# Kernel tuning notes

Hardware: AMD Instinct MI355X
Metric: run time of the kernel (lower is better)

## Reference

```python
import jax, jax.numpy as jnp
import numpy as np

B, S, H = 2, 2048, 2048
NH, KVH, HD = 16, 4, 128
R = 16
LORA_SCALE = 32.0 / 16.0  # lora_alpha / lora_r
ATTN_SCALE = HD ** -0.5
NEG = -1e9


def setup_inputs() -> dict:
    key = jax.random.key(0)
    ks = jax.random.split(key, 16)
    q_dim, kv_dim = NH * HD, KVH * HD
    # RoPE tables
    inv_freq = 1.0 / (10000.0 ** (jnp.arange(0, HD, 2, dtype=jnp.float32) / HD))
    ang = jnp.arange(S, dtype=jnp.float32)[:, None] * inv_freq[None, :]  # [S, HD/2]
    emb = jnp.concatenate([ang, ang], axis=-1)  # [S, HD]
    cos = jnp.broadcast_to(jnp.cos(emb)[None], (B, S, HD))
    sin = jnp.broadcast_to(jnp.sin(emb)[None], (B, S, HD))
    # additive causal mask [B,1,S,S]
    causal = jnp.triu(jnp.full((S, S), NEG, dtype=jnp.float32), k=1)
    attention_mask = jnp.broadcast_to(causal[None, None], (B, 1, S, S))
    return {
        'hidden_states': jax.random.normal(ks[0], (B, S, H), jnp.float32),
        'cos': cos,
        'sin': sin,
        'attention_mask': attention_mask,
        'q_w': jax.random.normal(ks[1], (q_dim, H), jnp.float32) * 0.02,
        'k_w': jax.random.normal(ks[2], (kv_dim, H), jnp.float32) * 0.02,
        'v_w': jax.random.normal(ks[3], (kv_dim, H), jnp.float32) * 0.02,
        'q_b': jax.random.normal(ks[4], (q_dim,), jnp.float32) * 0.02,
        'k_b': jax.random.normal(ks[5], (kv_dim,), jnp.float32) * 0.02,
        'v_b': jax.random.normal(ks[6], (kv_dim,), jnp.float32) * 0.02,
        'q_A': jax.random.normal(ks[7], (H, R), jnp.float32) * (1.0 / np.sqrt(H)),
        'q_B': jax.random.normal(ks[8], (R, q_dim), jnp.float32) * 0.02,
        'k_A': jax.random.normal(ks[9], (H, R), jnp.float32) * (1.0 / np.sqrt(H)),
        'k_B': jax.random.normal(ks[10], (R, kv_dim), jnp.float32) * 0.02,
        'v_A': jax.random.normal(ks[11], (H, R), jnp.float32) * (1.0 / np.sqrt(H)),
        'v_B': jax.random.normal(ks[12], (R, kv_dim), jnp.float32) * 0.02,
        'o_w': jax.random.normal(ks[13], (H, H), jnp.float32) * 0.02,
    }


def _rotate_half(x):
    x1, x2 = x[..., : HD // 2], x[..., HD // 2:]
    return jnp.concatenate([-x2, x1], axis=-1)


def reference(hidden_states, cos, sin, attention_mask,
              q_w, k_w, v_w, q_b, k_b, v_b,
              q_A, q_B, k_A, k_B, v_A, v_B, o_w):
    x = hidden_states  # dropout p=0 (eval)
    # fused base + LoRA projections
    q = x @ q_w.T + q_b + LORA_SCALE * ((x @ q_A) @ q_B)  # [B,S,NH*HD]
    k = x @ k_w.T + k_b + LORA_SCALE * ((x @ k_A) @ k_B)  # [B,S,KVH*HD]
    v = x @ v_w.T + v_b + LORA_SCALE * ((x @ v_A) @ v_B)
    q = q.reshape(B, S, NH, HD).transpose(0, 2, 1, 3)   # [B,NH,S,HD]
    k = k.reshape(B, S, KVH, HD).transpose(0, 2, 1, 3)  # [B,KVH,S,HD]
    v = v.reshape(B, S, KVH, HD).transpose(0, 2, 1, 3)
    # RoPE
    c = cos[:, None]  # [B,1,S,HD]
    s = sin[:, None]
    q = q * c + _rotate_half(q) * s
    k = k * c + _rotate_half(k) * s
    # GQA: repeat kv heads
    n_rep = NH // KVH
    k = jnp.repeat(k, n_rep, axis=1)  # [B,NH,S,HD]
    v = jnp.repeat(v, n_rep, axis=1)
    scores = jnp.einsum('bhqd,bhkd->bhqk', q, k) * ATTN_SCALE
    scores = scores + attention_mask
    attn = jax.nn.softmax(scores.astype(jnp.float32), axis=-1).astype(q.dtype)
    out = jnp.einsum('bhqk,bhkd->bhqd', attn, v)
    out = out.transpose(0, 2, 1, 3).reshape(B, S, NH * HD)  # [B,S,H]
    return out @ o_w.T
```

## Files before the change

### kernel.cpp

```cpp
#include <hip/hip_runtime.h>

constexpr int cB   = 2;
constexpr int cS   = 2048;
constexpr int cH   = 2048;
constexpr int cNH  = 16;
constexpr int cKVH = 4;
constexpr int cHD  = 128;
constexpr int cQD  = 2048;
constexpr int cKVD = 512;
constexpr int cNQKV = 3072;
constexpr int cNTOK = 4096;
#define ATTN_SCALE 0.08838834764831845f

typedef __bf16 bf16;
typedef __attribute__((ext_vector_type(8))) __bf16 bf16x8;
typedef __attribute__((ext_vector_type(4))) __bf16 bf16x4;
typedef __attribute__((ext_vector_type(4))) float  f32x4;

__device__ __forceinline__ void async_load16(const bf16* g, bf16* l) {
    __builtin_amdgcn_global_load_lds(
        (const __attribute__((address_space(1))) void*)g,
        (__attribute__((address_space(3))) void*)l, 16, 0, 0);
}

__global__ void conv_f32_bf16(const float* __restrict__ in, bf16* __restrict__ out) {
    int i = (blockIdx.x * 256 + threadIdx.x) * 4;
    f32x4 v = *(const f32x4*)(in + i);
    bf16x4 o;
    o[0] = (bf16)v[0]; o[1] = (bf16)v[1]; o[2] = (bf16)v[2]; o[3] = (bf16)v[3];
    *(bf16x4*)(out + i) = o;
}

__global__ void prep_w(const float* __restrict__ qw, const float* __restrict__ kw, const float* __restrict__ vw,
                       const float* __restrict__ qA, const float* __restrict__ qB,
                       const float* __restrict__ kA, const float* __restrict__ kB,
                       const float* __restrict__ vA, const float* __restrict__ vB,
                       bf16* __restrict__ Wc) {
    const int idx = blockIdx.x * 256 + threadIdx.x;
    const int n = idx >> 11, k = idx & 2047;
    const float* W; const float* Am; const float* Bm; int nn, nd;
    if (n < cQD)             { W = qw; Am = qA; Bm = qB; nn = n;          nd = cQD; }
    else if (n < cQD + cKVD) { W = kw; Am = kA; Bm = kB; nn = n - cQD;    nd = cKVD; }
    else                     { W = vw; Am = vA; Bm = vB; nn = n - cQD - cKVD; nd = cKVD; }
    float acc = 0.f;
    #pragma unroll
    for (int r = 0; r < 16; ++r) acc += Am[k * 16 + r] * Bm[r * nd + nn];
    Wc[(size_t)n * cH + k] = (bf16)(W[(size_t)nn * cH + k] + 2.0f * acc);
}

__global__ void prep_bias(const float* __restrict__ qb, const float* __restrict__ kb,
                          const float* __restrict__ vb, float* __restrict__ biasc) {
    int n = blockIdx.x * 256 + threadIdx.x;
    if (n >= cNQKV) return;
    biasc[n] = (n < cQD) ? qb[n] : (n < cQD + cKVD ? kb[n - cQD] : vb[n - cQD - cKVD]);
}

template <int OUTF32>
__global__ __launch_bounds__(256) void gemm_bt(const bf16* __restrict__ A, const bf16* __restrict__ Bw,
                                               const float* __restrict__ bias, void* __restrict__ Cp,
                                               int M, int N, int K) {
    __shared__ bf16 Al[128 * 32];
    __shared__ bf16 Bl[128 * 32];
    const int tid = threadIdx.x;
    const int wave = tid >> 6, lane = tid & 63;
    const int quad = lane >> 4, l16 = lane & 15;
    const int wr = wave >> 1, wc = wave & 1;
    const long bm = (long)blockIdx.y * 128, bn = (long)blockIdx.x * 128;

    f32x4 acc[4][4];
    #pragma unroll
    for (int i = 0; i < 4; ++i)
        #pragma unroll
        for (int c = 0; c < 4; ++c) acc[i][c] = f32x4{0.f, 0.f, 0.f, 0.f};

    const int r0 = lane >> 2;
    const int kc = (lane & 3) * 8;

    for (int k0 = 0; k0 < K; k0 += 32) {
        __syncthreads();
        #pragma unroll
        for (int j = 0; j < 2; ++j) {
            const int rb = (wave * 2 + j) * 16;
            const int row = rb + r0;
            async_load16(A  + (size_t)(bm + row) * K + k0 + kc, &Al[rb * 32 + r0 * 32 + kc]);
            async_load16(Bw + (size_t)(bn + row) * K + k0 + kc, &Bl[rb * 32 + r0 * 32 + kc]);
        }
        __syncthreads();
        bf16x8 af[4], bfr[4];
        #pragma unroll
        for (int i = 0; i < 4; ++i) af[i]  = *(const bf16x8*)&Al[(wr * 64 + i * 16 + l16) * 32 + quad * 8];
        #pragma unroll
        for (int c = 0; c < 4; ++c) bfr[c] = *(const bf16x8*)&Bl[(wc * 64 + c * 16 + l16) * 32 + quad * 8];
        #pragma unroll
        for (int i = 0; i < 4; ++i)
            #pragma unroll
            for (int c = 0; c < 4; ++c)
                acc[i][c] = __builtin_amdgcn_mfma_f32_16x16x32_bf16(af[i], bfr[c], acc[i][c], 0, 0, 0);
    }

    #pragma unroll
    for (int i = 0; i < 4; ++i)
        #pragma unroll
        for (int c = 0; c < 4; ++c) {
            const long m0 = bm + wr * 64 + i * 16 + quad * 4;
            const long n  = bn + wc * 64 + c * 16 + l16;
            #pragma unroll
            for (int r = 0; r < 4; ++r) {
                float v = acc[i][c][r];
                if (OUTF32) {
                    ((float*)Cp)[(m0 + r) * N + n] = v;
                } else {
                    v += bias[n];
                    ((bf16*)Cp)[(m0 + r) * N + n] = (bf16)v;
                }
            }
        }
}

__global__ void rope_reorder(const bf16* __restrict__ Y, const float* __restrict__ cosb,
                             const float* __restrict__ sinb,
                             bf16* __restrict__ Qr, bf16* __restrict__ Kr) {
    const int c = blockIdx.x * 256 + threadIdx.x;
    const int t = blockIdx.y;
    const int b = t >> 11, s = t & 2047;
    const int hh = c >> 6, dl = c & 63;
    const int col = hh * 128 + dl;
    const size_t yrow = (size_t)t * cNQKV;
    float y1 = (float)Y[yrow + col];
    float y2 = (float)Y[yrow + col + 64];
    float cv = cosb[(size_t)t * cHD + dl];
    float sv = sinb[(size_t)t * cHD + dl];
    float o1 = y1 * cv - y2 * sv;
    float o2 = y2 * cv + y1 * sv;
    if (hh < cNH) {
        o1 *= ATTN_SCALE; o2 *= ATTN_SCALE;
        bf16* dst = Qr + ((size_t)(b * cNH + hh) * cS + s) * cHD + dl;
        dst[0]  = (bf16)o1;
        dst[64] = (bf16)o2;
    } else {
        bf16* dst = Kr + ((size_t)(b * cKVH + (hh - cNH)) * cS + s) * cHD + dl;
        dst[0]  = (bf16)o1;
        dst[64] = (bf16)o2;
    }
}

__global__ void transpose_v(const bf16* __restrict__ Yq, bf16* __restrict__ Vt) {
    __shared__ bf16 tile[64 * 72];
    const int tid = threadIdx.x;
    const int stile = blockIdx.x;
    const int y = blockIdx.y;
    const int b = blockIdx.z;
    const int kv = y >> 1, dh = y & 1;
    const int r = tid >> 3, c8 = tid & 7;
    #pragma unroll
    for (int it = 0; it < 2; ++it) {
        int row = it * 32 + r;
        const bf16* src = Yq + ((size_t)(b * cS + stile * 64 + row)) * cNQKV
                          + cQD + cKVD + kv * cHD + dh * 64 + c8 * 8;
        *(bf16x8*)&tile[row * 72 + c8 * 8] = *(const bf16x8*)src;
    }
    __syncthreads();
    #pragma unroll
    for (int it = 0; it < 2; ++it) {
        int dr = it * 32 + r;
        bf16x8 o;
        #pragma unroll
        for (int j = 0; j < 8; ++j) o[j] = tile[(c8 * 8 + j) * 72 + dr];
        bf16* dst = Vt + ((size_t)((b * cKVH + kv) * cHD) + dh * 64 + dr) * cS + stile * 64 + c8 * 8;
        *(bf16x8*)dst = o;
    }
}

__global__ __launch_bounds__(256, 4) void flash3(const bf16* __restrict__ Q, const bf16* __restrict__ K,
                                                 const bf16* __restrict__ Vt, bf16* __restrict__ Ob) {
    __shared__ bf16 kb[8192];
    __shared__ bf16 vb[8192];
    __shared__ bf16 pb[4096];
    const int tid = threadIdx.x;
    const int wave = tid >> 6, lane = tid & 63;
    const int quad = lane >> 4, l16 = lane & 15;
    const int qt = (gridDim.x - 1) - blockIdx.x;
    const int h = blockIdx.y, b = blockIdx.z;

    const bf16* Qg = Q  + ((size_t)(b * cNH + h) * cS + qt * 64) * cHD;
    const bf16* Kg = K  + (size_t)(b * cKVH + (h >> 2)) * cS * cHD;
    const bf16* Vg = Vt + (size_t)(b * cKVH + (h >> 2)) * cHD * cS;

    bf16x8 qf[4];
    #pragma unroll
    for (int ks = 0; ks < 4; ++ks)
        qf[ks] = *(const bf16x8*)(Qg + (size_t)(wave * 16 + l16) * cHD + ks * 32 + quad * 8);

    int kgo[4], vgo[4], slo[4];
    #pragma unroll
    for (int i2 = 0; i2 < 4; ++i2) {
        const int si = i2 * 256 + tid;
        const int krow = si >> 4, kcsw = si & 15;
        const int kc = (kcsw & 8) | ((kcsw & 7) ^ (krow & 7));
        kgo[i2] = krow * cHD + kc * 8;
        const int vrow = si >> 3, vcsw = si & 7;
        const int vc = vcsw ^ (vrow & 7);
        vgo[i2] = vrow * cS + vc * 8;
        slo[i2] = si * 8;
    }

    f32x4 oac[8];
    #pragma unroll
    for (int dt = 0; dt < 8; ++dt) oac[dt] = f32x4{0.f, 0.f, 0.f, 0.f};
    float m_ = -3.0e38f, l_ = 0.f;

    const int nkt = qt + 1;
    for (int kt = 0; kt < nkt; ++kt) {
        __syncthreads();
        const bf16* Kt  = Kg + (size_t)kt * 64 * cHD;
        const bf16* Vtt = Vg + kt * 64;
        #pragma unroll
        for (int i2 = 0; i2 < 4; ++i2) async_load16(Kt + kgo[i2], kb + slo[i2]);
        #pragma unroll
        for (int i2 = 0; i2 < 4; ++i2) async_load16(Vtt + vgo[i2], vb + slo[i2]);
        __syncthreads();

        f32x4 st[4];
        #pragma unroll
        for (int mt = 0; mt < 4; ++mt) {
            bf16x8 kf[4];
            #pragma unroll
            for (int ks = 0; ks < 4; ++ks) {
                const int c = ks * 4 + quad;
                const int csw = (c & 8) | ((c & 7) ^ (l16 & 7));
                kf[ks] = *(const bf16x8*)&kb[(mt * 16 + l16) * 128 + csw * 8];
            }
            f32x4 a = f32x4{0.f, 0.f, 0.f, 0.f};
            #pragma unroll
            for (int ks = 0; ks < 4; ++ks)
                a = __builtin_amdgcn_mfma_f32_16x16x32_bf16(kf[ks], qf[ks], a, 0, 0, 0);
            st[mt] = a;
        }

        const int qpos = qt * 64 + wave * 16 + l16;
        const bool dm = (kt * 64 + 63) > (qt * 64 + wave * 16);
        float tmax = -3.0e38f;
        #pragma unroll
        for (int mt = 0; mt < 4; ++mt)
            #pragma unroll
            for (int r = 0; r < 4; ++r) {
                float v = st[mt][r];
                if (dm) {
                    const int kpos = kt * 64 + mt * 16 + quad * 4 + r;
                    if (kpos > qpos) v = -3.0e38f;
                }
                st[mt][r] = v;
                tmax = fmaxf(tmax, v);
            }
        tmax = fmaxf(tmax, __shfl_xor(tmax, 16, 64));
        tmax = fmaxf(tmax, __shfl_xor(tmax, 32, 64));
        const float mnew = fmaxf(m_, tmax);
        const float alpha = __expf(m_ - mnew);
        m_ = mnew;
        float rs = 0.f;
        #pragma unroll
        for (int mt = 0; mt < 4; ++mt)
            #pragma unroll
            for (int r = 0; r < 4; ++r) {
                const float p = __expf(st[mt][r] - mnew);
                st[mt][r] = p;
                rs += p;
            }
        rs += __shfl_xor(rs, 16, 64);
        rs += __shfl_xor(rs, 32, 64);
        l_ = l_ * alpha + rs;
        #pragma unroll
        for (int dt = 0; dt < 8; ++dt)
            #pragma unroll
            for (int r = 0; r < 4; ++r) oac[dt][r] *= alpha;

        #pragma unroll
        for (int mt = 0; mt < 4; ++mt) {
            bf16x4 p4;
            #pragma unroll
            for (int r = 0; r < 4; ++r) p4[r] = (bf16)st[mt][r];
            const int csw = (mt * 2 + (quad >> 1)) ^ (l16 & 7);
            *(bf16x4*)&pb[wave * 1024 + l16 * 64 + csw * 8 + (quad & 1) * 4] = p4;
        }

        bf16x8 pf[2];
        #pragma unroll
        for (int ks = 0; ks < 2; ++ks) {
            const int c = ks * 4 + quad;
            const int csw = c ^ (l16 & 7);
            pf[ks] = *(const bf16x8*)&pb[wave * 1024 + l16 * 64 + csw * 8];
        }
        #pragma unroll
        for (int dt = 0; dt < 8; ++dt) {
            bf16x8 vf[2];
            #pragma unroll
            for (int ks = 0; ks < 2; ++ks) {
                const int c = ks * 4 + quad;
                const int csw = c ^ (l16 & 7);
                vf[ks] = *(const bf16x8*)&vb[(dt * 16 + l16) * 64 + csw * 8];
            }
            #pragma unroll
            for (int ks = 0; ks < 2; ++ks)
                oac[dt] = __builtin_amdgcn_mfma_f32_16x16x32_bf16(vf[ks], pf[ks], oac[dt], 0, 0, 0);
        }
    }

    const float inv = 1.0f / l_;
    const int token = qt * 64 + wave * 16 + l16;
    bf16* orow = Ob + (size_t)(b * cS + token) * (cNH * cHD) + h * cHD;
    #pragma unroll
    for (int dt = 0; dt < 8; ++dt) {
        bf16x4 o4;
        #pragma unroll
        for (int r = 0; r < 4; ++r) o4[r] = (bf16)(oac[dt][r] * inv);
        *(bf16x4*)&orow[dt * 16 + quad * 4] = o4;
    }
}

extern "C" void kernel_launch(void* const* d_in, const int* in_sizes, int n_in,
                              void* d_out, int out_size, void* d_ws, size_t ws_size,
                              hipStream_t stream) {
    const float* x    = (const float*)d_in[0];
    const float* cosb = (const float*)d_in[1];
    const float* sinb = (const float*)d_in[2];
    const float* qw = (const float*)d_in[4];
    const float* kw = (const float*)d_in[5];
    const float* vw = (const float*)d_in[6];
    const float* qb = (const float*)d_in[7];
    const float* kb_ = (const float*)d_in[8];
    const float* vb = (const float*)d_in[9];
    const float* qA = (const float*)d_in[10];
    const float* qB = (const float*)d_in[11];
    const float* kA = (const float*)d_in[12];
    const float* kB = (const float*)d_in[13];
    const float* vA = (const float*)d_in[14];
    const float* vB = (const float*)d_in[15];
    const float* ow = (const float*)d_in[16];
    float* out = (float*)d_out;

    char* ws = (char*)d_ws;
    bf16* Xbf   = (bf16*)ws;  ws += (size_t)cNTOK * cH * 2;
    bf16* Wc    = (bf16*)ws;  ws += (size_t)cNQKV * cH * 2;
    float* biasc = (float*)ws; ws += (size_t)cNQKV * 4;
    bf16* Yq    = (bf16*)ws;  ws += (size_t)cNTOK * cNQKV * 2;
    bf16* Qr    = (bf16*)ws;  ws += (size_t)cB * cNH * cS * cHD * 2;
    bf16* Kr    = (bf16*)ws;  ws += (size_t)cB * cKVH * cS * cHD * 2;
    bf16* Vt    = (bf16*)ws;  ws += (size_t)cB * cKVH * cHD * cS * 2;
    bf16* OWbf  = (bf16*)ws;  ws += (size_t)cH * cH * 2;
    bf16* Aout  = Yq;

    conv_f32_bf16<<<(cNTOK * cH) / 1024, 256, 0, stream>>>(x, Xbf);
    conv_f32_bf16<<<(cH * cH) / 1024, 256, 0, stream>>>(ow, OWbf);
    prep_w<<<(cNQKV * cH) / 256, 256, 0, stream>>>(qw, kw, vw, qA, qB, kA, kB, vA, vB, Wc);
    prep_bias<<<(cNQKV + 255) / 256, 256, 0, stream>>>(qb, kb_, vb, biasc);

    gemm_bt<0><<<dim3(cNQKV / 128, cNTOK / 128), 256, 0, stream>>>(Xbf, Wc, biasc, (void*)Yq, cNTOK, cNQKV, cH);

    rope_reorder<<<dim3(5, cNTOK), 256, 0, stream>>>(Yq, cosb, sinb, Qr, Kr);
    transpose_v<<<dim3(cS / 64, 8, cB), 256, 0, stream>>>(Yq, Vt);

    flash3<<<dim3(cS / 64, cNH, cB), 256, 0, stream>>>(Qr, Kr, Vt, Aout);

    gemm_bt<1><<<dim3(cH / 128, cNTOK / 128), 256, 0, stream>>>(Aout, OWbf, nullptr, (void*)out, cNTOK, cH, cH);
}
```

Measured before the change: 434.5 us.

## Fuse RoPE and V transpose into QKV GEMM epilogue; pair causal tiles in flash

The QKV GEMM now adds bias, applies RoPE and the attention scale, and writes Q/K in head-major layout and V transposed directly from registers. This removes the intermediate Yq buffer and the separate rope_reorder and transpose_v kernels. The B-fragment column mapping is permuted so each wave holds both halves (d and d+64) of a head. The flash kernel now processes two query tiles per block (qt and 31-qt) to balance causal work, with a lower occupancy bound. Epilogue stores become scattered 2-byte writes, and the lower occupancy may reduce latency hiding.

```diff
diff --git a/kernel.cpp b/kernel.cpp
--- a/kernel.cpp
+++ b/kernel.cpp
@@ -55,10 +55,11 @@
     biasc[n] = (n < cQD) ? qb[n] : (n < cQD + cKVD ? kb[n - cQD] : vb[n - cQD - cKVD]);
 }
 
-template <int OUTF32>
-__global__ __launch_bounds__(256) void gemm_bt(const bf16* __restrict__ A, const bf16* __restrict__ Bw,
-                                               const float* __restrict__ bias, void* __restrict__ Cp,
-                                               int M, int N, int K) {
+__global__ __launch_bounds__(256) void gemm_qkv(const bf16* __restrict__ A, const bf16* __restrict__ Bw,
+                                                const float* __restrict__ bias,
+                                                const float* __restrict__ cosb, const float* __restrict__ sinb,
+                                                bf16* __restrict__ Qr, bf16* __restrict__ Kr,
+                                                bf16* __restrict__ Vt) {
     __shared__ bf16 Al[128 * 32];
     __shared__ bf16 Bl[128 * 32];
     const int tid = threadIdx.x;
@@ -66,6 +67,7 @@
     const int quad = lane >> 4, l16 = lane & 15;
     const int wr = wave >> 1, wc = wave & 1;
     const long bm = (long)blockIdx.y * 128, bn = (long)blockIdx.x * 128;
+    const int K = cH;
 
     f32x4 acc[4][4];
     #pragma unroll
@@ -90,6 +92,104 @@
         #pragma unroll
         for (int i = 0; i < 4; ++i) af[i]  = *(const bf16x8*)&Al[(wr * 64 + i * 16 + l16) * 32 + quad * 8];
         #pragma unroll
+        for (int c = 0; c < 4; ++c) {
+            const int nrow = wc * 32 + (c & 1) * 16 + (c >> 1) * 64 + l16;
+            bfr[c] = *(const bf16x8*)&Bl[nrow * 32 + quad * 8];
+        }
+        #pragma unroll
+        for (int i = 0; i < 4; ++i)
+            #pragma unroll
+            for (int c = 0; c < 4; ++c)
+                acc[i][c] = __builtin_amdgcn_mfma_f32_16x16x32_bf16(af[i], bfr[c], acc[i][c], 0, 0, 0);
+    }
+
+    #pragma unroll
+    for (int c = 0; c < 4; ++c) {
+        const int nloc = wc * 32 + (c & 1) * 16 + (c >> 1) * 64 + l16;
+        const float bv = bias[bn + nloc];
+        #pragma unroll
+        for (int i = 0; i < 4; ++i)
+            #pragma unroll
+            for (int r = 0; r < 4; ++r) acc[i][c][r] += bv;
+    }
+
+    const int head = (int)(bn >> 7);
+    if (head < cNH + cKVH) {
+        const bool isQ = head < cNH;
+        #pragma unroll
+        for (int cl = 0; cl < 2; ++cl) {
+            const int d = wc * 32 + cl * 16 + l16;
+            #pragma unroll
+            for (int i = 0; i < 4; ++i)
+                #pragma unroll
+                for (int r = 0; r < 4; ++r) {
+                    const long t = bm + wr * 64 + i * 16 + quad * 4 + r;
+                    const float cv = cosb[t * cHD + d];
+                    const float sv = sinb[t * cHD + d];
+                    const float v1 = acc[i][cl][r], v2 = acc[i][cl + 2][r];
+                    float o1 = v1 * cv - v2 * sv;
+                    float o2 = v2 * cv + v1 * sv;
+                    if (isQ) { o1 *= ATTN_SCALE; o2 *= ATTN_SCALE; }
+                    const int b = (int)(t >> 11), s = (int)(t & 2047);
+                    bf16* dst = isQ
+                        ? Qr + ((size_t)(b * cNH + head) * cS + s) * cHD
+                        : Kr + ((size_t)(b * cKVH + (head - cNH)) * cS + s) * cHD;
+                    dst[d]      = (bf16)o1;
+                    dst[d + 64] = (bf16)o2;
+                }
+        }
+    } else {
+        const int kv = head - cNH - cKVH;
+        const int b = (int)(bm >> 11);
+        const int sbase = (int)(bm & 2047);
+        #pragma unroll
+        for (int c = 0; c < 4; ++c) {
+            const int d = wc * 32 + (c & 1) * 16 + (c >> 1) * 64 + l16;
+            #pragma unroll
+            for (int i = 0; i < 4; ++i) {
+                const int s0 = sbase + wr * 64 + i * 16 + quad * 4;
+                bf16x4 o4;
+                #pragma unroll
+                for (int r = 0; r < 4; ++r) o4[r] = (bf16)acc[i][c][r];
+                *(bf16x4*)&Vt[((size_t)((b * cKVH + kv) * cHD) + d) * cS + s0] = o4;
+            }
+        }
+    }
+}
+
+__global__ __launch_bounds__(256) void gemm_bt_f32(const bf16* __restrict__ A, const bf16* __restrict__ Bw,
+                                                   float* __restrict__ Cp, int M, int N, int K) {
+    __shared__ bf16 Al[128 * 32];
+    __shared__ bf16 Bl[128 * 32];
+    const int tid = threadIdx.x;
+    const int wave = tid >> 6, lane = tid & 63;
+    const int quad = lane >> 4, l16 = lane & 15;
+    const int wr = wave >> 1, wc = wave & 1;
+    const long bm = (long)blockIdx.y * 128, bn = (long)blockIdx.x * 128;
+
+    f32x4 acc[4][4];
+    #pragma unroll
+    for (int i = 0; i < 4; ++i)
+        #pragma unroll
+        for (int c = 0; c < 4; ++c) acc[i][c] = f32x4{0.f, 0.f, 0.f, 0.f};
+
+    const int r0 = lane >> 2;
+    const int kc = (lane & 3) * 8;
+
+    for (int k0 = 0; k0 < K; k0 += 32) {
+        __syncthreads();
+        #pragma unroll
+        for (int j = 0; j < 2; ++j) {
+            const int rb = (wave * 2 + j) * 16;
+            const int row = rb + r0;
+            async_load16(A  + (size_t)(bm + row) * K + k0 + kc, &Al[rb * 32 + r0 * 32 + kc]);
+            async_load16(Bw + (size_t)(bn + row) * K + k0 + kc, &Bl[rb * 32 + r0 * 32 + kc]);
+        }
+        __syncthreads();
+        bf16x8 af[4], bfr[4];
+        #pragma unroll
+        for (int i = 0; i < 4; ++i) af[i]  = *(const bf16x8*)&Al[(wr * 64 + i * 16 + l16) * 32 + quad * 8];
+        #pragma unroll
         for (int c = 0; c < 4; ++c) bfr[c] = *(const bf16x8*)&Bl[(wc * 64 + c * 16 + l16) * 32 + quad * 8];
         #pragma unroll
         for (int i = 0; i < 4; ++i)
@@ -105,73 +205,12 @@
             const long m0 = bm + wr * 64 + i * 16 + quad * 4;
             const long n  = bn + wc * 64 + c * 16 + l16;
             #pragma unroll
-            for (int r = 0; r < 4; ++r) {
-                float v = acc[i][c][r];
-                if (OUTF32) {
-                    ((float*)Cp)[(m0 + r) * N + n] = v;
-                } else {
-                    v += bias[n];
-                    ((bf16*)Cp)[(m0 + r) * N + n] = (bf16)v;
-                }
-            }
-        }
-}
-
-__global__ void rope_reorder(const bf16* __restrict__ Y, const float* __restrict__ cosb,
-                             const float* __restrict__ sinb,
-                             bf16* __restrict__ Qr, bf16* __restrict__ Kr) {
-    const int c = blockIdx.x * 256 + threadIdx.x;
-    const int t = blockIdx.y;
-    const int b = t >> 11, s = t & 2047;
-    const int hh = c >> 6, dl = c & 63;
-    const int col = hh * 128 + dl;
-    const size_t yrow = (size_t)t * cNQKV;
-    float y1 = (float)Y[yrow + col];
-    float y2 = (float)Y[yrow + col + 64];
-    float cv = cosb[(size_t)t * cHD + dl];
-    float sv = sinb[(size_t)t * cHD + dl];
-    float o1 = y1 * cv - y2 * sv;
-    float o2 = y2 * cv + y1 * sv;
-    if (hh < cNH) {
-        o1 *= ATTN_SCALE; o2 *= ATTN_SCALE;
-        bf16* dst = Qr + ((size_t)(b * cNH + hh) * cS + s) * cHD + dl;
-        dst[0]  = (bf16)o1;
-        dst[64] = (bf16)o2;
-    } else {
-        bf16* dst = Kr + ((size_t)(b * cKVH + (hh - cNH)) * cS + s) * cHD + dl;
-        dst[0]  = (bf16)o1;
-        dst[64] = (bf16)o2;
-    }
-}
-
-__global__ void transpose_v(const bf16* __restrict__ Yq, bf16* __restrict__ Vt) {
-    __shared__ bf16 tile[64 * 72];
-    const int tid = threadIdx.x;
-    const int stile = blockIdx.x;
-    const int y = blockIdx.y;
-    const int b = blockIdx.z;
-    const int kv = y >> 1, dh = y & 1;
-    const int r = tid >> 3, c8 = tid & 7;
-    #pragma unroll
-    for (int it = 0; it < 2; ++it) {
-        int row = it * 32 + r;
-        const bf16* src = Yq + ((size_t)(b * cS + stile * 64 + row)) * cNQKV
-                          + cQD + cKVD + kv * cHD + dh * 64 + c8 * 8;
-        *(bf16x8*)&tile[row * 72 + c8 * 8] = *(const bf16x8*)src;
-    }
-    __syncthreads();
-    #pragma unroll
-    for (int it = 0; it < 2; ++it) {
-        int dr = it * 32 + r;
-        bf16x8 o;
-        #pragma unroll
-        for (int j = 0; j < 8; ++j) o[j] = tile[(c8 * 8 + j) * 72 + dr];
-        bf16* dst = Vt + ((size_t)((b * cKVH + kv) * cHD) + dh * 64 + dr) * cS + stile * 64 + c8 * 8;
-        *(bf16x8*)dst = o;
-    }
-}
-
-__global__ __launch_bounds__(256, 4) void flash3(const bf16* __restrict__ Q, const bf16* __restrict__ K,
+            for (int r = 0; r < 4; ++r)
+                Cp[(m0 + r) * N + n] = acc[i][c][r];
+        }
+}
+
+__global__ __launch_bounds__(256, 2) void flash4(const bf16* __restrict__ Q, const bf16* __restrict__ K,
                                                  const bf16* __restrict__ Vt, bf16* __restrict__ Ob) {
     __shared__ bf16 kb[8192];
     __shared__ bf16 vb[8192];
@@ -179,17 +218,12 @@
     const int tid = threadIdx.x;
     const int wave = tid >> 6, lane = tid & 63;
     const int quad = lane >> 4, l16 = lane & 15;
-    const int qt = (gridDim.x - 1) - blockIdx.x;
+    const int pi = blockIdx.x;
     const int h = blockIdx.y, b = blockIdx.z;
 
-    const bf16* Qg = Q  + ((size_t)(b * cNH + h) * cS + qt * 64) * cHD;
+    const bf16* Qh = Q  + (size_t)(b * cNH + h) * cS * cHD;
     const bf16* Kg = K  + (size_t)(b * cKVH + (h >> 2)) * cS * cHD;
     const bf16* Vg = Vt + (size_t)(b * cKVH + (h >> 2)) * cHD * cS;
-
-    bf16x8 qf[4];
-    #pragma unroll
-    for (int ks = 0; ks < 4; ++ks)
-        qf[ks] = *(const bf16x8*)(Qg + (size_t)(wave * 16 + l16) * cHD + ks * 32 + quad * 8);
 
     int kgo[4], vgo[4], slo[4];
     #pragma unroll
@@ -204,116 +238,127 @@
         slo[i2] = si * 8;
     }
 
-    f32x4 oac[8];
-    #pragma unroll
-    for (int dt = 0; dt < 8; ++dt) oac[dt] = f32x4{0.f, 0.f, 0.f, 0.f};
-    float m_ = -3.0e38f, l_ = 0.f;
-
-    const int nkt = qt + 1;
-    for (int kt = 0; kt < nkt; ++kt) {
-        __syncthreads();
-        const bf16* Kt  = Kg + (size_t)kt * 64 * cHD;
-        const bf16* Vtt = Vg + kt * 64;
-        #pragma unroll
-        for (int i2 = 0; i2 < 4; ++i2) async_load16(Kt + kgo[i2], kb + slo[i2]);
-        #pragma unroll
-        for (int i2 = 0; i2 < 4; ++i2) async_load16(Vtt + vgo[i2], vb + slo[i2]);
-        __syncthreads();
-
-        f32x4 st[4];
-        #pragma unroll
-        for (int mt = 0; mt < 4; ++mt) {
-            bf16x8 kf[4];
-            #pragma unroll
-            for (int ks = 0; ks < 4; ++ks) {
-                const int c = ks * 4 + quad;
-                const int csw = (c & 8) | ((c & 7) ^ (l16 & 7));
-                kf[ks] = *(const bf16x8*)&kb[(mt * 16 + l16) * 128 + csw * 8];
+    #pragma unroll
+    for (int t2 = 0; t2 < 2; ++t2) {
+        const int qt = t2 == 0 ? (31 - pi) : pi;
+
+        const bf16* Qg = Qh + (size_t)qt * 64 * cHD;
+        bf16x8 qf[4];
+        #pragma unroll
+        for (int ks = 0; ks < 4; ++ks)
+            qf[ks] = *(const bf16x8*)(Qg + (size_t)(wave * 16 + l16) * cHD + ks * 32 + quad * 8);
+
+        f32x4 oac[8];
+        #pragma unroll
+        for (int dt = 0; dt < 8; ++dt) oac[dt] = f32x4{0.f, 0.f, 0.f, 0.f};
+        float m_ = -3.0e38f, l_ = 0.f;
+
+        const int nkt = qt + 1;
+        for (int kt = 0; kt < nkt; ++kt) {
+            __syncthreads();
+            const bf16* Kt  = Kg + (size_t)kt * 64 * cHD;
+            const bf16* Vtt = Vg + kt * 64;
+            #pragma unroll
+            for (int i2 = 0; i2 < 4; ++i2) async_load16(Kt + kgo[i2], kb + slo[i2]);
+            #pragma unroll
+            for (int i2 = 0; i2 < 4; ++i2) async_load16(Vtt + vgo[i2], vb + slo[i2]);
+            __syncthreads();
+
+            f32x4 st[4];
+            #pragma unroll
+            for (int mt = 0; mt < 4; ++mt) {
+                bf16x8 kf[4];
+                #pragma unroll
+                for (int ks = 0; ks < 4; ++ks) {
+                    const int c = ks * 4 + quad;
+                    const int csw = (c & 8) | ((c & 7) ^ (l16 & 7));
+                    kf[ks] = *(const bf16x8*)&kb[(mt * 16 + l16) * 128 + csw * 8];
+                }
+                f32x4 a = f32x4{0.f, 0.f, 0.f, 0.f};
+                #pragma unroll
+                for (int ks = 0; ks < 4; ++ks)
+                    a = __builtin_amdgcn_mfma_f32_16x16x32_bf16(kf[ks], qf[ks], a, 0, 0, 0);
+                st[mt] = a;
             }
-            f32x4 a = f32x4{0.f, 0.f, 0.f, 0.f};
-            #pragma unroll
-            for (int ks = 0; ks < 4; ++ks)
-                a = __builtin_amdgcn_mfma_f32_16x16x32_bf16(kf[ks], qf[ks], a, 0, 0, 0);
-            st[mt] = a;
-        }
-
-        const int qpos = qt * 64 + wave * 16 + l16;
-        const bool dm = (kt * 64 + 63) > (qt * 64 + wave * 16);
-        float tmax = -3.0e38f;
-        #pragma unroll
-        for (int mt = 0; mt < 4; ++mt)
-            #pragma unroll
-            for (int r = 0; r < 4; ++r) {
-                float v = st[mt][r];
-                if (dm) {
-                    const int kpos = kt * 64 + mt * 16 + quad * 4 + r;
-                    if (kpos > qpos) v = -3.0e38f;
+
+            const int qpos = qt * 64 + wave * 16 + l16;
+            const bool dm = (kt * 64 + 63) > (qt * 64 + wave * 16);
+            float tmax = -3.0e38f;
+            #pragma unroll
+            for (int mt = 0; mt < 4; ++mt)
+                #pragma unroll
+                for (int r = 0; r < 4; ++r) {
+                    float v = st[mt][r];
+                    if (dm) {
+                        const int kpos = kt * 64 + mt * 16 + quad * 4 + r;
+                        if (kpos > qpos) v = -3.0e38f;
+                    }
+                    st[mt][r] = v;
+                    tmax = fmaxf(tmax, v);
                 }
-                st[mt][r] = v;
-                tmax = fmaxf(tmax, v);
+            tmax = fmaxf(tmax, __shfl_xor(tmax, 16, 64));
+            tmax = fmaxf(tmax, __shfl_xor(tmax, 32, 64));
+            const float mnew = fmaxf(m_, tmax);
+            const float alpha = __expf(m_ - mnew);
+            m_ = mnew;
+            float rs = 0.f;
+            #pragma unroll
+            for (int mt = 0; mt < 4; ++mt)
+                #pragma unroll
+                for (int r = 0; r < 4; ++r) {
+                    const float p = __expf(st[mt][r] - mnew);
+                    st[mt][r] = p;
+                    rs += p;
+                }
+            rs += __shfl_xor(rs, 16, 64);
+            rs += __shfl_xor(rs, 32, 64);
+            l_ = l_ * alpha + rs;
+            #pragma unroll
+            for (int dt = 0; dt < 8; ++dt)
+                #pragma unroll
+                for (int r = 0; r < 4; ++r) oac[dt][r] *= alpha;
+
+            #pragma unroll
+            for (int mt = 0; mt < 4; ++mt) {
+                bf16x4 p4;
+                #pragma unroll
+                for (int r = 0; r < 4; ++r) p4[r] = (bf16)st[mt][r];
+                const int csw = (mt * 2 + (quad >> 1)) ^ (l16 & 7);
+                *(bf16x4*)&pb[wave * 1024 + l16 * 64 + csw * 8 + (quad & 1) * 4] = p4;
             }
-        tmax = fmaxf(tmax, __shfl_xor(tmax, 16, 64));
-        tmax = fmaxf(tmax, __shfl_xor(tmax, 32, 64));
-        const float mnew = fmaxf(m_, tmax);
-        const float alpha = __expf(m_ - mnew);
-        m_ = mnew;
-        float rs = 0.f;
-        #pragma unroll
-        for (int mt = 0; mt < 4; ++mt)
-            #pragma unroll
-            for (int r = 0; r < 4; ++r) {
-                const float p = __expf(st[mt][r] - mnew);
-                st[mt][r] = p;
-                rs += p;
-            }
-        rs += __shfl_xor(rs, 16, 64);
-        rs += __shfl_xor(rs, 32, 64);
-        l_ = l_ * alpha + rs;
-        #pragma unroll
-        for (int dt = 0; dt < 8; ++dt)
-            #pragma unroll
-            for (int r = 0; r < 4; ++r) oac[dt][r] *= alpha;
-
-        #pragma unroll
-        for (int mt = 0; mt < 4; ++mt) {
-            bf16x4 p4;
-            #pragma unroll
-            for (int r = 0; r < 4; ++r) p4[r] = (bf16)st[mt][r];
-            const int csw = (mt * 2 + (quad >> 1)) ^ (l16 & 7);
-            *(bf16x4*)&pb[wave * 1024 + l16 * 64 + csw * 8 + (quad & 1) * 4] = p4;
-        }
-
-        bf16x8 pf[2];
-        #pragma unroll
-        for (int ks = 0; ks < 2; ++ks) {
-            const int c = ks * 4 + quad;
-            const int csw = c ^ (l16 & 7);
-            pf[ks] = *(const bf16x8*)&pb[wave * 1024 + l16 * 64 + csw * 8];
-        }
-        #pragma unroll
-        for (int dt = 0; dt < 8; ++dt) {
-            bf16x8 vf[2];
+
+            bf16x8 pf[2];
             #pragma unroll
             for (int ks = 0; ks < 2; ++ks) {
                 const int c = ks * 4 + quad;
                 const int csw = c ^ (l16 & 7);
-                vf[ks] = *(const bf16x8*)&vb[(dt * 16 + l16) * 64 + csw * 8];
+                pf[ks] = *(const bf16x8*)&pb[wave * 1024 + l16 * 64 + csw * 8];
             }
             #pragma unroll
-            for (int ks = 0; ks < 2; ++ks)
-                oac[dt] = __builtin_amdgcn_mfma_f32_16x16x32_bf16(vf[ks], pf[ks], oac[dt], 0, 0, 0);
-        }
-    }
-
-    const float inv = 1.0f / l_;
-    const int token = qt * 64 + wave * 16 + l16;
-    bf16* orow = Ob + (size_t)(b * cS + token) * (cNH * cHD) + h * cHD;
-    #pragma unroll
-    for (int dt = 0; dt < 8; ++dt) {
-        bf16x4 o4;
-        #pragma unroll
-        for (int r = 0; r < 4; ++r) o4[r] = (bf16)(oac[dt][r] * inv);
-        *(bf16x4*)&orow[dt * 16 + quad * 4] = o4;
+            for (int dt = 0; dt < 8; ++dt) {
+                bf16x8 vf[2];
+                #pragma unroll
+                for (int ks = 0; ks < 2; ++ks) {
+                    const int c = ks * 4 + quad;
+                    const int csw = c ^ (l16 & 7);
+                    vf[ks] = *(const bf16x8*)&vb[(dt * 16 + l16) * 64 + csw * 8];
+                }
+                #pragma unroll
+                for (int ks = 0; ks < 2; ++ks)
+                    oac[dt] = __builtin_amdgcn_mfma_f32_16x16x32_bf16(vf[ks], pf[ks], oac[dt], 0, 0, 0);
+            }
+        }
+
+        const float inv = 1.0f / l_;
+        const int token = qt * 64 + wave * 16 + l16;
+        bf16* orow = Ob + (size_t)(b * cS + token) * (cNH * cHD) + h * cHD;
+        #pragma unroll
+        for (int dt = 0; dt < 8; ++dt) {
+            bf16x4 o4;
+            #pragma unroll
+            for (int r = 0; r < 4; ++r) o4[r] = (bf16)(oac[dt][r] * inv);
+            *(bf16x4*)&orow[dt * 16 + quad * 4] = o4;
+        }
     }
 }
 
@@ -342,24 +387,20 @@
     bf16* Xbf   = (bf16*)ws;  ws += (size_t)cNTOK * cH * 2;
     bf16* Wc    = (bf16*)ws;  ws += (size_t)cNQKV * cH * 2;
     float* biasc = (float*)ws; ws += (size_t)cNQKV * 4;
-    bf16* Yq    = (bf16*)ws;  ws += (size_t)cNTOK * cNQKV * 2;
     bf16* Qr    = (bf16*)ws;  ws += (size_t)cB * cNH * cS * cHD * 2;
     bf16* Kr    = (bf16*)ws;  ws += (size_t)cB * cKVH * cS * cHD * 2;
     bf16* Vt    = (bf16*)ws;  ws += (size_t)cB * cKVH * cHD * cS * 2;
     bf16* OWbf  = (bf16*)ws;  ws += (size_t)cH * cH * 2;
-    bf16* Aout  = Yq;
+    bf16* Aout  = (bf16*)ws;  ws += (size_t)cNTOK * cQD * 2;
 
     conv_f32_bf16<<<(cNTOK * cH) / 1024, 256, 0, stream>>>(x, Xbf);
     conv_f32_bf16<<<(cH * cH) / 1024, 256, 0, stream>>>(ow, OWbf);
     prep_w<<<(cNQKV * cH) / 256, 256, 0, stream>>>(qw, kw, vw, qA, qB, kA, kB, vA, vB, Wc);
     prep_bias<<<(cNQKV + 255) / 256, 256, 0, stream>>>(qb, kb_, vb, biasc);
 
-    gemm_bt<0><<<dim3(cNQKV / 128, cNTOK / 128), 256, 0, stream>>>(Xbf, Wc, biasc, (void*)Yq, cNTOK, cNQKV, cH);
-
-    rope_reorder<<<dim3(5, cNTOK), 256, 0, stream>>>(Yq, cosb, sinb, Qr, Kr);
-    transpose_v<<<dim3(cS / 64, 8, cB), 256, 0, stream>>>(Yq, Vt);
-
-    flash3<<<dim3(cS / 64, cNH, cB), 256, 0, stream>>>(Qr, Kr, Vt, Aout);
-
-    gemm_bt<1><<<dim3(cH / 128, cNTOK / 128), 256, 0, stream>>>(Aout, OWbf, nullptr, (void*)out, cNTOK, cH, cH);
-}
+    gemm_qkv<<<dim3(cNQKV / 128, cNTOK / 128), 256, 0, stream>>>(Xbf, Wc, biasc, cosb, sinb, Qr, Kr, Vt);
+
+    flash4<<<dim3(16, cNH, cB), 256, 0, stream>>>(Qr, Kr, Vt, Aout);
+
+    gemm_bt_f32<<<dim3(cH / 128, cNTOK / 128), 256, 0, stream>>>(Aout, OWbf, out, cNTOK, cH, cH);
+}
```

New measurement: 406.8 us. -6.4%, faster.
